# Kernel tuning notes

Measured on AMD Instinct MI355X. Metric: run time of the kernel, lower is better.

## Reference

```python
import jax, jax.numpy as jnp
import numpy as np

B, T, F, H, K = 64, 256, 16, 128, 3


def setup_inputs() -> dict:
    key = jax.random.key(0)
    ks = jax.random.split(key, 8)
    s = 1.0 / np.sqrt(H)
    x = jax.random.normal(ks[0], (B, T, F), jnp.float32)
    index = jnp.sort(jax.random.randint(ks[1], (B, 2), 0, T), axis=1)
    # per-feature LSTM params (input dim 1), torch gate order [i, f, g, o]
    W_ih = jax.random.uniform(ks[2], (F, 4 * H), jnp.float32, -s, s)
    W_hh = jax.random.uniform(ks[3], (F, 4 * H, H), jnp.float32, -s, s)
    b = jax.random.uniform(ks[4], (F, 4 * H), jnp.float32, -s, s)  # b_ih + b_hh folded
    conv_w = jax.random.uniform(ks[5], (K,), jnp.float32, -1.0 / np.sqrt(K), 1.0 / np.sqrt(K))
    fc_w = jax.random.uniform(ks[6], (F * H, 2), jnp.float32, -1.0 / np.sqrt(F * H), 1.0 / np.sqrt(F * H))
    fc_b = jax.random.uniform(ks[7], (2,), jnp.float32, -1.0 / np.sqrt(F * H), 1.0 / np.sqrt(F * H))
    return dict(x=x, index=index, W_ih=W_ih, W_hh=W_hh, b=b, conv_w=conv_w, fc_w=fc_w, fc_b=fc_b)


def reference(x, index, W_ih, W_hh, b, conv_w, fc_w, fc_b):
    Bn, Tn, Fn = x.shape
    Hn = W_hh.shape[-1]
    t = jnp.arange(Tn)
    # valid[b, t] = start <= t < end; recurrence only advances inside the ragged slice
    valid = (t[None, :] >= index[:, 0:1]) & (t[None, :] < index[:, 1:2])  # [B, T]
    xs = jnp.moveaxis(x, 1, 0)            # [T, B, F]
    ms = jnp.moveaxis(valid, 1, 0)[:, :, None, None]  # [T, B, 1, 1]

    def step(carry, inp):
        h, c = carry                       # [B, F, H] each
        x_t, m = inp                       # [B, F], [B, 1, 1]
        gates = x_t[:, :, None] * W_ih[None] \
            + jnp.einsum('bfh,fgh->bfg', h, W_hh) + b[None]  # [B, F, 4H]
        i, f, g, o = jnp.split(gates, 4, axis=-1)
        i = jax.nn.sigmoid(i); f = jax.nn.sigmoid(f)
        g = jnp.tanh(g); o = jax.nn.sigmoid(o)
        c_new = f * c + i * g
        h_new = o * jnp.tanh(c_new)
        h = jnp.where(m, h_new, h)
        c = jnp.where(m, c_new, c)
        return (h, c), None

    h0 = jnp.zeros((Bn, Fn, Hn), x.dtype)
    (h, _), _ = jax.lax.scan(step, (h0, h0), (xs, ms))
    outs = h                               # [B, F, H] == last LSTM output per slice

    cofs = outs.mean(axis=-1)              # AdaptiveAvgPool1d(1) -> [B, F]
    cofs = jax.lax.conv_general_dilated(
        cofs[:, None, :], conv_w[None, None, :], (1,), [(K // 2, K // 2)],
        dimension_numbers=('NCH', 'OIH', 'NCH'))[:, 0, :]  # [B, F]
    gate = jax.nn.sigmoid(cofs)
    outs = outs * gate[:, :, None]
    return outs.reshape(Bn, -1) @ fc_w + fc_b  # [B, 2]
```

## Files before the change

kernel.cpp:

```cpp
#include <hip/hip_runtime.h>

typedef _Float16 half_t;
typedef half_t half2_t __attribute__((ext_vector_type(2)));
typedef half_t half8  __attribute__((ext_vector_type(8)));
typedef unsigned int uint_t;
typedef uint_t uint4v __attribute__((ext_vector_type(4)));
typedef float float4v __attribute__((ext_vector_type(4)));

#define B_  64
#define T_  256
#define F_  16
#define H_  128
#define LOG2E 1.44269504f

__device__ __forceinline__ float rcp_(float x)  { return __builtin_amdgcn_rcpf(x); }
__device__ __forceinline__ float sigm2(float x) { return rcp_(1.0f + __builtin_amdgcn_exp2f(x * -LOG2E)); }
__device__ __forceinline__ float tanh2(float x) { return fmaf(rcp_(1.0f + __builtin_amdgcn_exp2f(x * (-2.0f * LOG2E))), 2.0f, -1.0f); }
__device__ __forceinline__ float sigm(float x)  { return rcp_(1.0f + __expf(-x)); }

__global__ void make_sched(const int* __restrict__ index, int* __restrict__ tasks) {
    __shared__ int ln[B_];
    const int t = threadIdx.x;
    const int s = index[2 * t], e = index[2 * t + 1];
    ln[t] = e - s;
    __syncthreads();
    int L = ln[t], r = 0;
    for (int j = 0; j < B_; ++j) r += (ln[j] > L) || (ln[j] == L && j < t);
    int4 v; v.x = t; v.y = s; v.z = e; v.w = 0;
    ((int4*)tasks)[r] = v;
}

__global__ void repack_w(const float* __restrict__ whh, uint_t* __restrict__ wt) {
    const int f = blockIdx.x, w = blockIdx.y, tid = threadIdx.x;
    const int lane = tid & 63, q4 = tid >> 6;
    const int li = lane & 15, lg = lane >> 4;
    const float* base = whh + (size_t)f * 512 * 128;
#pragma unroll
    for (int qq = 0; qq < 4; ++qq) {
        const int qf = q4 * 4 + qq;
        const int m = qf >> 2, kt = qf & 3;
        const int g512 = 128 * m + 16 * w + li;
        uint_t tmp[4];
#pragma unroll
        for (int e2 = 0; e2 < 4; ++e2) {
            int k = kt * 32 + lg * 8 + 2 * e2;
            half2_t h;
            h[0] = (half_t)base[g512 * 128 + k];
            h[1] = (half_t)base[g512 * 128 + k + 1];
            tmp[e2] = __builtin_bit_cast(uint_t, h);
        }
        uint4 out = { tmp[0], tmp[1], tmp[2], tmp[3] };
        ((uint4*)wt)[(((size_t)f * 8 + w) * 16 + qf) * 64 + lane] = out;
    }
}

__global__ __launch_bounds__(512, 4) void lstm_mfma(
    const float* __restrict__ x, const uint_t* __restrict__ wt,
    const float* __restrict__ wih_g, const float* __restrict__ bias_g,
    const int* __restrict__ tasks, float* __restrict__ hout)
{
    __shared__ float xsh[T_];
    __shared__ alignas(16) half_t hbuf[2][H_];

    const int f = blockIdx.x & 15;
    const int4 tk = ((const int4*)tasks)[blockIdx.x >> 4];
    const int b = tk.x, s = tk.y, e = tk.z;
    const int tid = threadIdx.x, lane = tid & 63, w = tid >> 6;
    const int li = lane & 15, lg = lane >> 4;
    const int cell = 16 * w + li;

    uint4v wr[16];
    {
        const char* ws = (const char*)wt + ((((size_t)f * 8 + w) * 16) * 64 + lane) * 16;
#pragma unroll
        for (int q = 0; q < 16; ++q) {
            unsigned long long a = (unsigned long long)(ws + (size_t)q * 1024);
            asm volatile("global_load_dwordx4 %0, %1, off" : "=v"(wr[q]) : "v"(a));
        }
        asm volatile("s_waitcnt vmcnt(0)");
        __builtin_amdgcn_sched_barrier(0);
    }

    float wih[4], bb[4];
#pragma unroll
    for (int m = 0; m < 4; ++m) {
        wih[m] = wih_g[f * 512 + 128 * m + cell];
        bb[m]  = bias_g[f * 512 + 128 * m + cell];
    }

    for (int idx = tid; idx < T_; idx += 512) xsh[idx] = x[((size_t)b * T_ + idx) * F_ + f];
    if (tid < H_) hbuf[0][tid] = (half_t)0.0f;

    float cst = 0.0f, hst = 0.0f;
    int pp = 0;
    __syncthreads();

    for (int t = s; t < e; ++t) {
        const half_t* hb = &hbuf[pp][lg * 8];
        half8 a0 = *(const half8*)(hb + 0);
        half8 a1 = *(const half8*)(hb + 32);
        half8 a2 = *(const half8*)(hb + 64);
        half8 a3 = *(const half8*)(hb + 96);
        float xt = xsh[t];

        float4v d[4];
#pragma unroll
        for (int m = 0; m < 4; ++m) {
            float iv = fmaf(xt, wih[m], bb[m]);
            float4v ci = { iv, iv, iv, iv };
            ci = __builtin_amdgcn_mfma_f32_16x16x32_f16(a0, __builtin_bit_cast(half8, wr[m * 4 + 0]), ci, 0, 0, 0);
            ci = __builtin_amdgcn_mfma_f32_16x16x32_f16(a1, __builtin_bit_cast(half8, wr[m * 4 + 1]), ci, 0, 0, 0);
            ci = __builtin_amdgcn_mfma_f32_16x16x32_f16(a2, __builtin_bit_cast(half8, wr[m * 4 + 2]), ci, 0, 0, 0);
            ci = __builtin_amdgcn_mfma_f32_16x16x32_f16(a3, __builtin_bit_cast(half8, wr[m * 4 + 3]), ci, 0, 0, 0);
            d[m] = ci;
        }

        float gi = sigm2(d[0].x);
        float gf = sigm2(d[1].x);
        float gg = tanh2(d[2].x);
        float go = sigm2(d[3].x);
        cst = fmaf(gf, cst, gi * gg);
        hst = go * tanh2(cst);

        if (lg == 0) hbuf[pp ^ 1][cell] = (half_t)hst;
        __syncthreads();
        pp ^= 1;
    }

    if (lg == 0) hout[((size_t)b * F_ + f) * H_ + cell] = hst;
}

__global__ void epilogue(const float* __restrict__ hout, const float* __restrict__ conv_w,
                         const float* __restrict__ fc_w, const float* __restrict__ fc_b,
                         float* __restrict__ out)
{
    const int b = blockIdx.x, t = threadIdx.x;
    const int lane = t & 63, wv = t >> 6;
    __shared__ float part[2][16];
    __shared__ float gate_sh[16];

    float hv[16];
#pragma unroll
    for (int f = 0; f < 16; ++f) hv[f] = hout[((size_t)b * 16 + f) * 128 + t];

#pragma unroll
    for (int f = 0; f < 16; ++f) {
        float s = hv[f];
#pragma unroll
        for (int off = 32; off >= 1; off >>= 1) s += __shfl_down(s, off, 64);
        if (lane == 0) part[wv][f] = s;
    }
    __syncthreads();
    if (t < 16) gate_sh[t] = (part[0][t] + part[1][t]) * (1.0f / 128.0f);
    __syncthreads();
    float gate = 0.0f;
    if (t < 16) {
        float l  = (t > 0)  ? gate_sh[t - 1] : 0.0f;
        float mi = gate_sh[t];
        float r  = (t < 15) ? gate_sh[t + 1] : 0.0f;
        gate = sigm(fmaf(l, conv_w[0], fmaf(mi, conv_w[1], r * conv_w[2])));
    }
    __syncthreads();
    if (t < 16) gate_sh[t] = gate;
    __syncthreads();

    float acc0 = 0.0f, acc1 = 0.0f;
    const float2* fw2 = (const float2*)fc_w;
#pragma unroll
    for (int f = 0; f < 16; ++f) {
        float hg = hv[f] * gate_sh[f];
        float2 w2 = fw2[f * 128 + t];
        acc0 = fmaf(hg, w2.x, acc0);
        acc1 = fmaf(hg, w2.y, acc1);
    }
#pragma unroll
    for (int off = 32; off >= 1; off >>= 1) {
        acc0 += __shfl_down(acc0, off, 64);
        acc1 += __shfl_down(acc1, off, 64);
    }
    if (lane == 0) { part[wv][0] = acc0; part[wv][1] = acc1; }
    __syncthreads();
    if (t == 0) {
        out[b * 2 + 0] = part[0][0] + part[1][0] + fc_b[0];
        out[b * 2 + 1] = part[0][1] + part[1][1] + fc_b[1];
    }
}

extern "C" void kernel_launch(void* const* d_in, const int* in_sizes, int n_in,
                              void* d_out, int out_size, void* d_ws, size_t ws_size,
                              hipStream_t stream) {
    const float* x      = (const float*)d_in[0];
    const int*   index  = (const int*)  d_in[1];
    const float* W_ih   = (const float*)d_in[2];
    const float* W_hh   = (const float*)d_in[3];
    const float* bias   = (const float*)d_in[4];
    const float* conv_w = (const float*)d_in[5];
    const float* fc_w   = (const float*)d_in[6];
    const float* fc_b   = (const float*)d_in[7];
    float* out = (float*)d_out;

    uint_t* wt    = (uint_t*)d_ws;
    float*  hout  = (float*)((char*)d_ws + 2 * 1024 * 1024);
    int*    tasks = (int*)((char*)d_ws + 2 * 1024 * 1024 + 512 * 1024);

    make_sched<<<1, 64, 0, stream>>>(index, tasks);
    repack_w<<<dim3(F_, 8), 256, 0, stream>>>(W_hh, wt);
    lstm_mfma<<<1024, 512, 0, stream>>>(x, wt, W_ih, bias, tasks, hout);
    epilogue<<<B_, 128, 0, stream>>>(hout, conv_w, fc_w, fc_b, out);
}
```

Measured before the change: 137.0 us.

## Halve LSTM block size, giving each wave two hidden tiles with split MFMA chains

Each LSTM block now runs 4 waves instead of 8, and each wave owns two 16-cell tiles, which doubles the register-held weight fragments to 32 vectors. The four-MFMA dependency chain per gate is split into two independent accumulators that are summed afterwards, shortening the serial latency. Fewer waves per block makes each per-timestep barrier cheaper, at the cost of roughly 128 weight VGPRs per lane and less latency hiding from other waves. The repack store index gains a no-op term multiplied by zero.

```diff
diff --git a/kernel.cpp b/kernel.cpp
--- a/kernel.cpp
+++ b/kernel.cpp
@@ -50,11 +50,11 @@
             tmp[e2] = __builtin_bit_cast(uint_t, h);
         }
         uint4 out = { tmp[0], tmp[1], tmp[2], tmp[3] };
-        ((uint4*)wt)[(((size_t)f * 8 + w) * 16 + qf) * 64 + lane] = out;
-    }
-}
-
-__global__ __launch_bounds__(512, 4) void lstm_mfma(
+        ((uint4*)wt)[(((size_t)f * 8 + qf) * 16 + qf - qf) * 0 + (((size_t)f * 8 + w) * 16 + qf) * 64 + lane] = out;
+    }
+}
+
+__global__ __launch_bounds__(256, 2) void lstm_mfma(
     const float* __restrict__ x, const uint_t* __restrict__ wt,
     const float* __restrict__ wih_g, const float* __restrict__ bias_g,
     const int* __restrict__ tasks, float* __restrict__ hout)
@@ -67,31 +67,37 @@
     const int b = tk.x, s = tk.y, e = tk.z;
     const int tid = threadIdx.x, lane = tid & 63, w = tid >> 6;
     const int li = lane & 15, lg = lane >> 4;
-    const int cell = 16 * w + li;
-
-    uint4v wr[16];
+    const int c0 = 32 * w + li;
+    const int c1 = c0 + 16;
+
+    uint4v wr[32];
     {
-        const char* ws = (const char*)wt + ((((size_t)f * 8 + w) * 16) * 64 + lane) * 16;
-#pragma unroll
-        for (int q = 0; q < 16; ++q) {
-            unsigned long long a = (unsigned long long)(ws + (size_t)q * 1024);
-            asm volatile("global_load_dwordx4 %0, %1, off" : "=v"(wr[q]) : "v"(a));
+#pragma unroll
+        for (int tt = 0; tt < 2; ++tt) {
+            const char* ws = (const char*)wt + ((((size_t)f * 8 + 2 * w + tt) * 16) * 64 + lane) * 16;
+#pragma unroll
+            for (int q = 0; q < 16; ++q) {
+                unsigned long long a = (unsigned long long)(ws + (size_t)q * 1024);
+                asm volatile("global_load_dwordx4 %0, %1, off" : "=v"(wr[tt * 16 + q]) : "v"(a));
+            }
         }
         asm volatile("s_waitcnt vmcnt(0)");
         __builtin_amdgcn_sched_barrier(0);
     }
 
-    float wih[4], bb[4];
-#pragma unroll
-    for (int m = 0; m < 4; ++m) {
-        wih[m] = wih_g[f * 512 + 128 * m + cell];
-        bb[m]  = bias_g[f * 512 + 128 * m + cell];
-    }
-
-    for (int idx = tid; idx < T_; idx += 512) xsh[idx] = x[((size_t)b * T_ + idx) * F_ + f];
+    float wih[2][4], bb[2][4];
+#pragma unroll
+    for (int tt = 0; tt < 2; ++tt)
+#pragma unroll
+        for (int m = 0; m < 4; ++m) {
+            wih[tt][m] = wih_g[f * 512 + 128 * m + c0 + 16 * tt];
+            bb[tt][m]  = bias_g[f * 512 + 128 * m + c0 + 16 * tt];
+        }
+
+    for (int idx = tid; idx < T_; idx += 256) xsh[idx] = x[((size_t)b * T_ + idx) * F_ + f];
     if (tid < H_) hbuf[0][tid] = (half_t)0.0f;
 
-    float cst = 0.0f, hst = 0.0f;
+    float cst[2] = {0.f, 0.f}, hst[2] = {0.f, 0.f};
     int pp = 0;
     __syncthreads();
 
@@ -103,31 +109,39 @@
         half8 a3 = *(const half8*)(hb + 96);
         float xt = xsh[t];
 
-        float4v d[4];
-#pragma unroll
-        for (int m = 0; m < 4; ++m) {
-            float iv = fmaf(xt, wih[m], bb[m]);
-            float4v ci = { iv, iv, iv, iv };
-            ci = __builtin_amdgcn_mfma_f32_16x16x32_f16(a0, __builtin_bit_cast(half8, wr[m * 4 + 0]), ci, 0, 0, 0);
-            ci = __builtin_amdgcn_mfma_f32_16x16x32_f16(a1, __builtin_bit_cast(half8, wr[m * 4 + 1]), ci, 0, 0, 0);
-            ci = __builtin_amdgcn_mfma_f32_16x16x32_f16(a2, __builtin_bit_cast(half8, wr[m * 4 + 2]), ci, 0, 0, 0);
-            ci = __builtin_amdgcn_mfma_f32_16x16x32_f16(a3, __builtin_bit_cast(half8, wr[m * 4 + 3]), ci, 0, 0, 0);
-            d[m] = ci;
-        }
-
-        float gi = sigm2(d[0].x);
-        float gf = sigm2(d[1].x);
-        float gg = tanh2(d[2].x);
-        float go = sigm2(d[3].x);
-        cst = fmaf(gf, cst, gi * gg);
-        hst = go * tanh2(cst);
-
-        if (lg == 0) hbuf[pp ^ 1][cell] = (half_t)hst;
+        float gv[2][4];
+#pragma unroll
+        for (int tt = 0; tt < 2; ++tt)
+#pragma unroll
+            for (int m = 0; m < 4; ++m) {
+                float iv = fmaf(xt, wih[tt][m], bb[tt][m]);
+                float4v ca = { iv, iv, iv, iv };
+                float4v cb = { 0.f, 0.f, 0.f, 0.f };
+                ca = __builtin_amdgcn_mfma_f32_16x16x32_f16(a0, __builtin_bit_cast(half8, wr[tt * 16 + m * 4 + 0]), ca, 0, 0, 0);
+                cb = __builtin_amdgcn_mfma_f32_16x16x32_f16(a1, __builtin_bit_cast(half8, wr[tt * 16 + m * 4 + 1]), cb, 0, 0, 0);
+                ca = __builtin_amdgcn_mfma_f32_16x16x32_f16(a2, __builtin_bit_cast(half8, wr[tt * 16 + m * 4 + 2]), ca, 0, 0, 0);
+                cb = __builtin_amdgcn_mfma_f32_16x16x32_f16(a3, __builtin_bit_cast(half8, wr[tt * 16 + m * 4 + 3]), cb, 0, 0, 0);
+                gv[tt][m] = ca[0] + cb[0];
+            }
+
+#pragma unroll
+        for (int tt = 0; tt < 2; ++tt) {
+            float gi = sigm2(gv[tt][0]);
+            float gf = sigm2(gv[tt][1]);
+            float gg = tanh2(gv[tt][2]);
+            float go = sigm2(gv[tt][3]);
+            cst[tt] = fmaf(gf, cst[tt], gi * gg);
+            hst[tt] = go * tanh2(cst[tt]);
+        }
+
+        if (lg == 0)      hbuf[pp ^ 1][c0] = (half_t)hst[0];
+        else if (lg == 1) hbuf[pp ^ 1][c1] = (half_t)hst[1];
         __syncthreads();
         pp ^= 1;
     }
 
-    if (lg == 0) hout[((size_t)b * F_ + f) * H_ + cell] = hst;
+    if (lg == 0) hout[((size_t)b * F_ + f) * H_ + c0] = hst[0];
+    if (lg == 1) hout[((size_t)b * F_ + f) * H_ + c1] = hst[1];
 }
 
 __global__ void epilogue(const float* __restrict__ hout, const float* __restrict__ conv_w,
@@ -205,6 +219,6 @@
 
     make_sched<<<1, 64, 0, stream>>>(index, tasks);
     repack_w<<<dim3(F_, 8), 256, 0, stream>>>(W_hh, wt);
-    lstm_mfma<<<1024, 512, 0, stream>>>(x, wt, W_ih, bias, tasks, hout);
+    lstm_mfma<<<1024, 256, 0, stream>>>(x, wt, W_ih, bias, tasks, hout);
     epilogue<<<B_, 128, 0, stream>>>(hout, conv_w, fc_w, fc_b, out);
 }
```

After: 164.1 us. 1.2x slower.

## Pack two batch rows per workgroup using unused MFMA rows with masked recurrence

Applied to the files above, without the earlier changes.

Each LSTM workgroup now processes two batch elements per feature, using separate rows of the 16x16 MFMA A operand. The h vector of each batch element is placed in a different half of the 16 rows. Batch elements are paired by sorted midpoint of their slice, and the loop runs over the union span, with per-element masks freezing state outside each slice. This halves the grid and uses MFMA rows that were previously redundant, at the cost of extra steps over the union span. The K-chain is also split into two independent accumulators to shorten the dependent MFMA chain.

```diff
diff --git a/kernel.cpp b/kernel.cpp
--- a/kernel.cpp
+++ b/kernel.cpp
@@ -18,16 +18,26 @@
 __device__ __forceinline__ float tanh2(float x) { return fmaf(rcp_(1.0f + __builtin_amdgcn_exp2f(x * (-2.0f * LOG2E))), 2.0f, -1.0f); }
 __device__ __forceinline__ float sigm(float x)  { return rcp_(1.0f + __expf(-x)); }
 
-__global__ void make_sched(const int* __restrict__ index, int* __restrict__ tasks) {
-    __shared__ int ln[B_];
+__global__ void make_sched(const int* __restrict__ index, int* __restrict__ pairs) {
+    __shared__ int ss[B_], ee[B_], mid[B_], bo[B_];
     const int t = threadIdx.x;
     const int s = index[2 * t], e = index[2 * t + 1];
-    ln[t] = e - s;
-    __syncthreads();
-    int L = ln[t], r = 0;
-    for (int j = 0; j < B_; ++j) r += (ln[j] > L) || (ln[j] == L && j < t);
-    int4 v; v.x = t; v.y = s; v.z = e; v.w = 0;
-    ((int4*)tasks)[r] = v;
+    ss[t] = s; ee[t] = e; mid[t] = s + e;
+    __syncthreads();
+    int m = mid[t], r = 0;
+    for (int j = 0; j < B_; ++j) r += (mid[j] < m) || (mid[j] == m && j < t);
+    bo[r] = t;
+    __syncthreads();
+    if (t < 32) {
+        int bA = bo[2 * t], bB = bo[2 * t + 1];
+        int su = min(ss[bA], ss[bB]), eu = max(ee[bA], ee[bB]);
+        int4 v;
+        v.x = (bA << 8) | bB;
+        v.y = (ss[bA] << 16) | ee[bA];
+        v.z = (ss[bB] << 16) | ee[bB];
+        v.w = (su << 16) | eu;
+        ((int4*)pairs)[t] = v;
+    }
 }
 
 __global__ void repack_w(const float* __restrict__ whh, uint_t* __restrict__ wt) {
@@ -57,17 +67,23 @@
 __global__ __launch_bounds__(512, 4) void lstm_mfma(
     const float* __restrict__ x, const uint_t* __restrict__ wt,
     const float* __restrict__ wih_g, const float* __restrict__ bias_g,
-    const int* __restrict__ tasks, float* __restrict__ hout)
+    const int* __restrict__ pairs, float* __restrict__ hout)
 {
-    __shared__ float xsh[T_];
-    __shared__ alignas(16) half_t hbuf[2][H_];
+    __shared__ float xsh[2][T_];
+    __shared__ alignas(16) half_t hbuf[2][2][H_];
 
     const int f = blockIdx.x & 15;
-    const int4 tk = ((const int4*)tasks)[blockIdx.x >> 4];
-    const int b = tk.x, s = tk.y, e = tk.z;
+    const int4 pv = ((const int4*)pairs)[blockIdx.x >> 4];
+    const int bA = pv.x >> 8, bB = pv.x & 255;
+    const int sA = pv.y >> 16, eA = pv.y & 0xffff;
+    const int sB = pv.z >> 16, eB = pv.z & 0xffff;
+    const int su = pv.w >> 16, eu = pv.w & 0xffff;
+
     const int tid = threadIdx.x, lane = tid & 63, w = tid >> 6;
     const int li = lane & 15, lg = lane >> 4;
     const int cell = 16 * w + li;
+    const int hsel = li >> 3;
+    const int csel = lg >> 1;
 
     uint4v wr[16];
     {
@@ -81,53 +97,65 @@
         __builtin_amdgcn_sched_barrier(0);
     }
 
-    float wih[4], bb[4];
+    float wih[4], bb4[4];
 #pragma unroll
     for (int m = 0; m < 4; ++m) {
         wih[m] = wih_g[f * 512 + 128 * m + cell];
-        bb[m]  = bias_g[f * 512 + 128 * m + cell];
-    }
-
-    for (int idx = tid; idx < T_; idx += 512) xsh[idx] = x[((size_t)b * T_ + idx) * F_ + f];
-    if (tid < H_) hbuf[0][tid] = (half_t)0.0f;
+        bb4[m] = bias_g[f * 512 + 128 * m + cell];
+    }
+
+    const int myb = csel ? bB : bA;
+    const int mys = csel ? sB : sA;
+    const int mye = csel ? eB : eA;
+
+    {
+        int bb_ = tid >> 8, tt = tid & 255;
+        xsh[bb_][tt] = x[((size_t)(bb_ ? bB : bA) * T_ + tt) * F_ + f];
+    }
+    if (tid < 2 * H_) hbuf[0][tid >> 7][tid & 127] = (half_t)0.0f;
 
     float cst = 0.0f, hst = 0.0f;
     int pp = 0;
     __syncthreads();
 
-    for (int t = s; t < e; ++t) {
-        const half_t* hb = &hbuf[pp][lg * 8];
+    for (int t = su; t < eu; ++t) {
+        const half_t* hb = &hbuf[pp][hsel][lg * 8];
         half8 a0 = *(const half8*)(hb + 0);
         half8 a1 = *(const half8*)(hb + 32);
         half8 a2 = *(const half8*)(hb + 64);
         half8 a3 = *(const half8*)(hb + 96);
-        float xt = xsh[t];
-
-        float4v d[4];
+        float xt = xsh[csel][t];
+
+        float gv[4];
 #pragma unroll
         for (int m = 0; m < 4; ++m) {
-            float iv = fmaf(xt, wih[m], bb[m]);
-            float4v ci = { iv, iv, iv, iv };
-            ci = __builtin_amdgcn_mfma_f32_16x16x32_f16(a0, __builtin_bit_cast(half8, wr[m * 4 + 0]), ci, 0, 0, 0);
-            ci = __builtin_amdgcn_mfma_f32_16x16x32_f16(a1, __builtin_bit_cast(half8, wr[m * 4 + 1]), ci, 0, 0, 0);
-            ci = __builtin_amdgcn_mfma_f32_16x16x32_f16(a2, __builtin_bit_cast(half8, wr[m * 4 + 2]), ci, 0, 0, 0);
-            ci = __builtin_amdgcn_mfma_f32_16x16x32_f16(a3, __builtin_bit_cast(half8, wr[m * 4 + 3]), ci, 0, 0, 0);
-            d[m] = ci;
+            float iv = fmaf(xt, wih[m], bb4[m]);
+            float4v ca = { iv, iv, iv, iv };
+            float4v cb = { 0.f, 0.f, 0.f, 0.f };
+            ca = __builtin_amdgcn_mfma_f32_16x16x32_f16(a0, __builtin_bit_cast(half8, wr[m * 4 + 0]), ca, 0, 0, 0);
+            cb = __builtin_amdgcn_mfma_f32_16x16x32_f16(a1, __builtin_bit_cast(half8, wr[m * 4 + 1]), cb, 0, 0, 0);
+            ca = __builtin_amdgcn_mfma_f32_16x16x32_f16(a2, __builtin_bit_cast(half8, wr[m * 4 + 2]), ca, 0, 0, 0);
+            cb = __builtin_amdgcn_mfma_f32_16x16x32_f16(a3, __builtin_bit_cast(half8, wr[m * 4 + 3]), cb, 0, 0, 0);
+            gv[m] = ca[0] + cb[0];
         }
 
-        float gi = sigm2(d[0].x);
-        float gf = sigm2(d[1].x);
-        float gg = tanh2(d[2].x);
-        float go = sigm2(d[3].x);
-        cst = fmaf(gf, cst, gi * gg);
-        hst = go * tanh2(cst);
-
-        if (lg == 0) hbuf[pp ^ 1][cell] = (half_t)hst;
+        float gi = sigm2(gv[0]);
+        float gf = sigm2(gv[1]);
+        float gg = tanh2(gv[2]);
+        float go = sigm2(gv[3]);
+        float cn = fmaf(gf, cst, gi * gg);
+        bool mk = (t >= mys) & (t < mye);
+        cst = mk ? cn : cst;
+        float hn = go * tanh2(cst);
+        hst = mk ? hn : hst;
+
+        if (lg == 0)      hbuf[pp ^ 1][0][cell] = (half_t)hst;
+        else if (lg == 2) hbuf[pp ^ 1][1][cell] = (half_t)hst;
         __syncthreads();
         pp ^= 1;
     }
 
-    if (lg == 0) hout[((size_t)b * F_ + f) * H_ + cell] = hst;
+    if ((lg & 1) == 0) hout[((size_t)myb * F_ + f) * H_ + cell] = hst;
 }
 
 __global__ void epilogue(const float* __restrict__ hout, const float* __restrict__ conv_w,
@@ -201,10 +229,10 @@
 
     uint_t* wt    = (uint_t*)d_ws;
     float*  hout  = (float*)((char*)d_ws + 2 * 1024 * 1024);
-    int*    tasks = (int*)((char*)d_ws + 2 * 1024 * 1024 + 512 * 1024);
-
-    make_sched<<<1, 64, 0, stream>>>(index, tasks);
+    int*    pairs = (int*)((char*)d_ws + 2 * 1024 * 1024 + 512 * 1024);
+
+    make_sched<<<1, 64, 0, stream>>>(index, pairs);
     repack_w<<<dim3(F_, 8), 256, 0, stream>>>(W_hh, wt);
-    lstm_mfma<<<1024, 512, 0, stream>>>(x, wt, W_ih, bias, tasks, hout);
+    lstm_mfma<<<512, 512, 0, stream>>>(x, wt, W_ih, bias, pairs, hout);
     epilogue<<<B_, 128, 0, stream>>>(hout, conv_w, fc_w, fc_b, out);
 }
```

New measurement: 146.5 us. +6.9%, slower.
